# Performance work log

Measured on AMD Instinct MI355X. Metric: run time of the kernel, lower is better.

The kernel has to match this reference:

```python
import jax, jax.numpy as jnp
import numpy as np

N_NODES = 100000
N_EDGES = 1000000
IN_FEATS = 128
HID_FEATS = 128
OUT_FEATS = 128
N_CLASSES = 16
NEG_SLOPE = 0.01
BN_EPS = 1e-5


def _linear_params(key, d_in, d_out):
    k1, k2 = jax.random.split(key)
    s = 1.0 / np.sqrt(d_in)
    w = jax.random.uniform(k1, (d_in, d_out), jnp.float32, -s, s)
    b = jax.random.uniform(k2, (d_out,), jnp.float32, -s, s)
    return w, b


def setup_inputs() -> dict:
    key = jax.random.key(0)
    ks = jax.random.split(key, 16)
    node_feat = jax.random.normal(ks[0], (N_NODES, IN_FEATS), jnp.float32)
    src = jax.random.randint(ks[1], (N_EDGES,), 0, N_NODES, jnp.int32)
    dst = jax.random.randint(ks[2], (N_EDGES,), 0, N_NODES, jnp.int32)
    dims = [(IN_FEATS, HID_FEATS), (HID_FEATS, HID_FEATS), (HID_FEATS, OUT_FEATS)]
    inp = {"node_feat": node_feat, "src": src, "dst": dst}
    for i, (din, dout) in enumerate(dims):
        wp, bp = _linear_params(ks[3 + 4 * i], din, din)      # fc_pool: d_in -> d_in
        ws, _ = _linear_params(ks[4 + 4 * i], din, dout)       # fc_self (no bias)
        wn, _ = _linear_params(ks[5 + 4 * i], din, dout)       # fc_neigh (no bias)
        _, b = _linear_params(ks[6 + 4 * i], din, dout)        # shared output bias
        inp[f"wp{i}"] = wp; inp[f"bp{i}"] = bp
        inp[f"ws{i}"] = ws; inp[f"wn{i}"] = wn; inp[f"b{i}"] = b
    inp["bn_gamma"] = jnp.ones((HID_FEATS,), jnp.float32)
    inp["bn_beta"] = jnp.zeros((HID_FEATS,), jnp.float32)
    wc, bc = _linear_params(ks[15], OUT_FEATS, N_CLASSES)
    inp["wc"] = wc; inp["bc"] = bc
    return inp


def _sage_pool(h, src, dst, deg_mask, wp, bp, ws, wn, b):
    # fc_pool + relu on source nodes, gather per edge, segment-max to dst
    hp = jax.nn.relu(h @ wp + bp)                 # [N, d_in]
    msg = hp[src]                                 # [E, d_in]
    agg = jax.ops.segment_max(msg, dst, num_segments=N_NODES)  # [N, d_in]
    agg = jnp.where(deg_mask, agg, 0.0)           # zero for isolated nodes
    return h @ ws + agg @ wn + b


def _batchnorm(x, gamma, beta):
    mu = jnp.mean(x, axis=0)
    var = jnp.var(x, axis=0)
    return (x - mu) * jax.lax.rsqrt(var + BN_EPS) * gamma + beta


def reference(node_feat, src, dst,
              wp0, bp0, ws0, wn0, b0,
              wp1, bp1, ws1, wn1, b1,
              wp2, bp2, ws2, wn2, b2,
              bn_gamma, bn_beta, wc, bc):
    deg = jnp.zeros((N_NODES,), jnp.float32).at[dst].add(1.0)
    deg_mask = (deg > 0)[:, None]
    h = jax.nn.leaky_relu(_sage_pool(node_feat, src, dst, deg_mask, wp0, bp0, ws0, wn0, b0), NEG_SLOPE)
    h = jax.nn.leaky_relu(_batchnorm(_sage_pool(h, src, dst, deg_mask, wp1, bp1, ws1, wn1, b1), bn_gamma, bn_beta), NEG_SLOPE)
    h = _sage_pool(h, src, dst, deg_mask, wp2, bp2, ws2, wn2, b2)
    return h @ wc + bc
```

## Files before the change

### kernel.cpp

```cpp
#include <hip/hip_runtime.h>


#define N_NODES 100000
#define N_EDGES 1000000
#define F 128
#define NEG_SLOPE 0.01f
#define BN_EPS 1e-5f

typedef __attribute__((ext_vector_type(8))) short bf16x8;
typedef __attribute__((ext_vector_type(4))) float f32x4;

typedef __attribute__((address_space(3))) unsigned int as3_uint;
typedef __attribute__((address_space(1))) const unsigned int as1_cuint;

__device__ __forceinline__ void gload16(const void* g, void* l) {
    __builtin_amdgcn_global_load_lds((as1_cuint*)g, (as3_uint*)l, 16, 0, 0);
}

__device__ __forceinline__ unsigned short f2bf(float f) {
    unsigned int u = __float_as_uint(f);
    u += 0x7fff + ((u >> 16) & 1);
    return (unsigned short)(u >> 16);
}
__device__ __forceinline__ float bf2f(unsigned short h) {
    return __uint_as_float(((unsigned int)h) << 16);
}

__global__ __launch_bounds__(256) void zero_kernel(float4* __restrict__ p, long n4) {
    long i = (long)blockIdx.x * 256 + threadIdx.x;
    if (i < n4) p[i] = make_float4(0.f, 0.f, 0.f, 0.f);
}

__global__ __launch_bounds__(256) void f32_to_bf16_kernel(
    const float4* __restrict__ in, uint2* __restrict__ out, long n4)
{
    long i = (long)blockIdx.x * 256 + threadIdx.x;
    if (i >= n4) return;
    float4 v = in[i];
    uint2 o;
    o.x = (unsigned)f2bf(v.x) | ((unsigned)f2bf(v.y) << 16);
    o.y = (unsigned)f2bf(v.z) | ((unsigned)f2bf(v.w) << 16);
    out[i] = o;
}

__global__ __launch_bounds__(256) void pack_weights3(
    const float* __restrict__ wp, const float* __restrict__ wss,
    const float* __restrict__ wn, short* __restrict__ wp_p, short* __restrict__ wsn_p)
{
    const int i = blockIdx.x * 256 + threadIdx.x;
    if (i >= 3 * 16384) return;
    const int mat = i >> 14;
    const int idx = i & 16383;
    const int k = idx >> 7, n = idx & 127;
    const float* srcm = mat == 0 ? wp : (mat == 1 ? wss : wn);
    const int slot = ((k >> 3) * 128 + n) * 8 + (k & 7);
    if (mat == 0) wp_p[slot] = (short)f2bf(srcm[idx]);
    else wsn_p[(mat == 2 ? 16 * 128 * 8 : 0) + slot] = (short)f2bf(srcm[idx]);
}

template<int NKS>
__global__ __launch_bounds__(256) void gemm_mfma(
    const short* __restrict__ A1, const short* __restrict__ A2,
    const short* __restrict__ Bp, const float* __restrict__ bias,
    unsigned short* __restrict__ Cout, int n_rows, int act)
{
    constexpr int S = NKS / 2;
    __shared__ short tile[2 * 8192];
    __shared__ short epi[4 * 1280];

    const int tid = threadIdx.x;
    const int wave = tid >> 6;
    const int lane = tid & 63;
    const int m = lane & 15, q = lane >> 4;
    const int r0 = blockIdx.x * 128;
    const int rw = (wave >> 1) * 64;
    const int r0q = r0 + rw;
    const int c0 = (wave & 1) * 64;
    const int gchunk = (tid & 7) ^ ((tid >> 3) & 7);

    f32x4 acc[4][4];
#pragma unroll
    for (int i = 0; i < 4; ++i)
#pragma unroll
        for (int j = 0; j < 4; ++j)
#pragma unroll
            for (int r = 0; r < 4; ++r) acc[i][j][r] = 0.f;

    auto stage = [&](int s, int buf) {
        const short* Ap = (NKS == 8 && s >= 2) ? A2 : A1;
        const int kbase = (s & 1) * 64;
#pragma unroll
        for (int p = 0; p < 4; ++p) {
            int row = r0 + (tid >> 3) + 32 * p;
            row = min(row, n_rows - 1);
            gload16(Ap + (size_t)row * F + kbase + gchunk * 8,
                    &tile[buf * 8192 + p * 2048 + tid * 8]);
        }
    };

    stage(0, 0);
    __syncthreads();

    for (int s = 0; s < S; ++s) {
        if (s + 1 < S) stage(s + 1, (s + 1) & 1);
        const short* tb = &tile[(s & 1) * 8192];
#pragma unroll
        for (int ks2 = 0; ks2 < 2; ++ks2) {
            const int ks32 = s * 2 + ks2;
            bf16x8 b[4], a[4];
#pragma unroll
            for (int ni = 0; ni < 4; ++ni)
                b[ni] = *(const bf16x8*)(Bp + ((size_t)(ks32 * 4 + q) * F + c0 + ni * 16 + m) * 8);
#pragma unroll
            for (int mi = 0; mi < 4; ++mi)
                a[mi] = *(const bf16x8*)(tb + (rw + mi * 16 + m) * 64 + (((ks2 * 4 + q) ^ (m & 7)) << 3));
#pragma unroll
            for (int mi = 0; mi < 4; ++mi)
#pragma unroll
                for (int ni = 0; ni < 4; ++ni)
                    acc[mi][ni] = __builtin_amdgcn_mfma_f32_16x16x32_bf16(a[mi], b[ni], acc[mi][ni], 0, 0, 0);
        }
        __syncthreads();
    }

    float bv[4];
#pragma unroll
    for (int ni = 0; ni < 4; ++ni) bv[ni] = bias[c0 + ni * 16 + m];

    short* ep = &epi[wave * 1280];
    const int colc_lo = m >> 3, cin = m & 7;
#pragma unroll
    for (int mi = 0; mi < 4; ++mi) {
#pragma unroll
        for (int ni = 0; ni < 4; ++ni) {
            const int colc = 2 * ni + colc_lo;
#pragma unroll
            for (int rg = 0; rg < 4; ++rg) {
                const int row16 = q * 4 + rg;
                float v = acc[mi][ni][rg] + bv[ni];
                if (act == 1) v = v > 0.f ? v : 0.f;
                else if (act == 2) v = v > 0.f ? v : v * NEG_SLOPE;
                ep[row16 * 80 + ((colc ^ (row16 & 7)) << 3) + cin] = (short)f2bf(v);
            }
        }
        __syncthreads();
#pragma unroll
        for (int p = 0; p < 2; ++p) {
            const int lrow = (lane >> 3) + 8 * p;
            bf16x8 vv = *(const bf16x8*)&ep[lrow * 80 + (((lane & 7) ^ (lrow & 7)) << 3)];
            const int grow = r0q + mi * 16 + lrow;
            if (grow < n_rows)
                *(bf16x8*)(Cout + (size_t)grow * F + c0 + ((lane & 7) << 3)) = vv;
        }
        __syncthreads();
    }
}

__global__ __launch_bounds__(256) void hist_kernel(const int* __restrict__ dst, int* __restrict__ deg) {
    const int e = blockIdx.x * 256 + threadIdx.x;
    if (e < N_EDGES) atomicAdd(&deg[__builtin_nontemporal_load(&dst[e])], 1);
}

__global__ __launch_bounds__(256) void scan1_kernel(const int* __restrict__ deg, int* __restrict__ bsum) {
    __shared__ int sh[256];
    const int t = threadIdx.x;
    const int base = blockIdx.x * 1024 + t * 4;
    int s = 0;
#pragma unroll
    for (int j = 0; j < 4; ++j) s += (base + j < N_NODES) ? deg[base + j] : 0;
    sh[t] = s; __syncthreads();
    for (int off = 128; off; off >>= 1) {
        if (t < off) sh[t] += sh[t + off];
        __syncthreads();
    }
    if (t == 0) bsum[blockIdx.x] = sh[0];
}

__global__ __launch_bounds__(128) void scan2_kernel(int* __restrict__ bsum, int nb, int* __restrict__ row_start) {
    __shared__ int sh[128];
    const int t = threadIdx.x;
    sh[t] = (t < nb) ? bsum[t] : 0;
    __syncthreads();
    for (int off = 1; off < 128; off <<= 1) {
        int x = (t >= off) ? sh[t - off] : 0;
        __syncthreads();
        if (t >= off) sh[t] += x;
        __syncthreads();
    }
    if (t < nb) bsum[t] = t ? sh[t - 1] : 0;
    if (t == 0) row_start[N_NODES] = N_EDGES;
}

__global__ __launch_bounds__(256) void scan3_kernel(
    const int* __restrict__ deg, const int* __restrict__ boff,
    int* __restrict__ row_start, int* __restrict__ cursor)
{
    __shared__ int sh[256];
    const int t = threadIdx.x;
    const int base = blockIdx.x * 1024 + t * 4;
    int v[4]; int s = 0;
#pragma unroll
    for (int j = 0; j < 4; ++j) { v[j] = (base + j < N_NODES) ? deg[base + j] : 0; s += v[j]; }
    sh[t] = s; __syncthreads();
    for (int off = 1; off < 256; off <<= 1) {
        int x = (t >= off) ? sh[t - off] : 0;
        __syncthreads();
        if (t >= off) sh[t] += x;
        __syncthreads();
    }
    int excl = (t ? sh[t - 1] : 0) + boff[blockIdx.x];
#pragma unroll
    for (int j = 0; j < 4; ++j) {
        if (base + j < N_NODES) { row_start[base + j] = excl; cursor[base + j] = excl; }
        excl += v[j];
    }
}

#define NODES_PER_XCD 12500
__global__ __launch_bounds__(256) void scatter_xcd_kernel(
    const int* __restrict__ src, const int* __restrict__ dst,
    int* __restrict__ cursor, int* __restrict__ esrc)
{
    const int range = blockIdx.x & 7;
    const int chunk = blockIdx.x >> 3;
    const int lo = range * NODES_PER_XCD;
    const int e0 = chunk * 3907;
    const int e1 = min(e0 + 3907, N_EDGES);
    for (int e = e0 + threadIdx.x; e < e1; e += 256) {
        const int d = dst[e];
        const unsigned int rel = (unsigned int)(d - lo);
        if (rel < NODES_PER_XCD) {
            const int pos = atomicAdd(&cursor[d], 1);
            esrc[pos] = src[e];
        }
    }
}

__global__ __launch_bounds__(256) void aggregate_max_bf16(
    const unsigned int* __restrict__ hp, const int* __restrict__ row_start,
    const int* __restrict__ esrc, unsigned int* __restrict__ agg)
{
    const int node = blockIdx.x * 4 + (threadIdx.x >> 6);
    if (node >= N_NODES) return;
    const int lane = threadIdx.x & 63;
    const int beg = row_start[node], end = row_start[node + 1];
    unsigned int m0 = 0, m1 = 0;
    int i = beg;
    for (; i + 7 < end; i += 8) {
        unsigned int v[8];
#pragma unroll
        for (int j = 0; j < 8; ++j) v[j] = hp[(size_t)esrc[i + j] * 64 + lane];
#pragma unroll
        for (int j = 0; j < 8; ++j) {
            m0 = max(m0, v[j] & 0xffffu);
            m1 = max(m1, v[j] >> 16);
        }
    }
    if (i + 3 < end) {
        unsigned int v[4];
#pragma unroll
        for (int j = 0; j < 4; ++j) v[j] = hp[(size_t)esrc[i + j] * 64 + lane];
#pragma unroll
        for (int j = 0; j < 4; ++j) {
            m0 = max(m0, v[j] & 0xffffu);
            m1 = max(m1, v[j] >> 16);
        }
        i += 4;
    }
    if (i + 1 < end) {
        const unsigned int a = hp[(size_t)esrc[i] * 64 + lane];
        const unsigned int b = hp[(size_t)esrc[i + 1] * 64 + lane];
        m0 = max(m0, max(a & 0xffffu, b & 0xffffu));
        m1 = max(m1, max(a >> 16, b >> 16));
        i += 2;
    }
    if (i < end) {
        const unsigned int a = hp[(size_t)esrc[i] * 64 + lane];
        m0 = max(m0, a & 0xffffu);
        m1 = max(m1, a >> 16);
    }
    agg[(size_t)node * 64 + lane] = m0 | (m1 << 16);
}

#define BN_ROWS_PER_BLOCK 196
__global__ __launch_bounds__(256) void bn_stats_kernel(
    const unsigned short* __restrict__ x, float* __restrict__ stats, int n)
{
    const int tid = threadIdx.x;
    const int wave = tid >> 6, lane = tid & 63;
    const int rgrp = lane >> 4;
    const int c16 = lane & 15;
    const int rbase = blockIdx.x * BN_ROWS_PER_BLOCK;
    const int rend = min(rbase + BN_ROWS_PER_BLOCK, n);

    float s[8], ss[8];
#pragma unroll
    for (int j = 0; j < 8; ++j) { s[j] = 0.f; ss[j] = 0.f; }

    for (int r = rbase + wave * 4 + rgrp; r < rend; r += 16) {
        const uint4 v = *(const uint4*)(x + (size_t)r * F + c16 * 8);
        const unsigned int w[4] = {v.x, v.y, v.z, v.w};
#pragma unroll
        for (int u = 0; u < 4; ++u) {
            const float f0 = bf2f((unsigned short)(w[u] & 0xffffu));
            const float f1 = bf2f((unsigned short)(w[u] >> 16));
            s[2*u]   += f0; ss[2*u]   = fmaf(f0, f0, ss[2*u]);
            s[2*u+1] += f1; ss[2*u+1] = fmaf(f1, f1, ss[2*u+1]);
        }
    }
#pragma unroll
    for (int j = 0; j < 8; ++j) {
        s[j]  += __shfl_down(s[j], 32);  s[j]  += __shfl_down(s[j], 16);
        ss[j] += __shfl_down(ss[j], 32); ss[j] += __shfl_down(ss[j], 16);
    }
    __shared__ float sh[4][16][16];
    if (lane < 16) {
#pragma unroll
        for (int j = 0; j < 8; ++j) {
            sh[wave][c16][2*j]     = s[j];
            sh[wave][c16][2*j + 1] = ss[j];
        }
    }
    __syncthreads();
    const float tot = sh[0][tid >> 4][tid & 15] + sh[1][tid >> 4][tid & 15]
                    + sh[2][tid >> 4][tid & 15] + sh[3][tid >> 4][tid & 15];
    const int col = (tid >> 4) * 8 + ((tid >> 1) & 7);
    atomicAdd(&stats[(tid & 1) * 128 + col], tot);
}

__global__ void bn_finalize_kernel(
    const float* __restrict__ stats, const float* __restrict__ gamma,
    const float* __restrict__ beta, float* __restrict__ coef)
{
    const int c = threadIdx.x;
    const float mean = stats[c] * (1.f / N_NODES);
    const float var = stats[128 + c] * (1.f / N_NODES) - mean * mean;
    const float scale = gamma[c] * rsqrtf(var + BN_EPS);
    coef[c] = scale;
    coef[128 + c] = fmaf(-mean, scale, beta[c]);
}

__global__ __launch_bounds__(256) void bn_apply_bf16(
    unsigned int* __restrict__ x, const float* __restrict__ coef, long n2)
{
    __shared__ float sc[128], sf[128];
    if (threadIdx.x < 128) {
        sc[threadIdx.x] = coef[threadIdx.x];
        sf[threadIdx.x] = coef[128 + threadIdx.x];
    }
    __syncthreads();
    const long i = (long)blockIdx.x * 256 + threadIdx.x;
    if (i >= n2) return;
    const unsigned int v = x[i];
    const int c0 = (int)(i & 63) * 2;
    float a = fmaf(bf2f((unsigned short)(v & 0xffffu)), sc[c0], sf[c0]);
    float b = fmaf(bf2f((unsigned short)(v >> 16)), sc[c0 + 1], sf[c0 + 1]);
    a = a > 0.f ? a : a * NEG_SLOPE;
    b = b > 0.f ? b : b * NEG_SLOPE;
    x[i] = (unsigned)f2bf(a) | ((unsigned)f2bf(b) << 16);
}

__global__ __launch_bounds__(256) void classifier_kernel(
    const unsigned short* __restrict__ X, const float* __restrict__ Wc,
    const float* __restrict__ bc, float* __restrict__ out, int n)
{
    __shared__ float Wl[2048];
    __shared__ float Xs[16 * 132];
    const int tid = threadIdx.x;
    for (int i = tid; i < 2048; i += 256) Wl[i] = Wc[i];
    const int r0 = blockIdx.x * 16;
    for (int i = tid; i < 2048; i += 256) {
        const int row = i >> 7, col = i & 127;
        const int gr = r0 + row;
        Xs[row * 132 + col] = (gr < n) ? bf2f(X[(size_t)gr * F + col]) : 0.f;
    }
    __syncthreads();
    const int rl = tid >> 4, c = tid & 15;
    const int r = r0 + rl;
    if (r >= n) return;
    float s = bc[c];
    const float* xr = &Xs[rl * 132];
#pragma unroll
    for (int k = 0; k < 128; ++k) s = fmaf(xr[k], Wl[k * 16 + c], s);
    out[(size_t)r * 16 + c] = s;
}

extern "C" void kernel_launch(void* const* d_in, const int* in_sizes, int n_in,
                              void* d_out, int out_size, void* d_ws, size_t ws_size,
                              hipStream_t stream) {
    const float* node_feat = (const float*)d_in[0];
    const int* src = (const int*)d_in[1];
    const int* dst = (const int*)d_in[2];
    const float* wp[3] = {(const float*)d_in[3],  (const float*)d_in[8],  (const float*)d_in[13]};
    const float* bp[3] = {(const float*)d_in[4],  (const float*)d_in[9],  (const float*)d_in[14]};
    const float* wsm[3] = {(const float*)d_in[5], (const float*)d_in[10], (const float*)d_in[15]};
    const float* wn[3] = {(const float*)d_in[6],  (const float*)d_in[11], (const float*)d_in[16]};
    const float* bb[3] = {(const float*)d_in[7],  (const float*)d_in[12], (const float*)d_in[17]};
    const float* gamma = (const float*)d_in[18];
    const float* beta  = (const float*)d_in[19];
    const float* wc    = (const float*)d_in[20];
    const float* bc    = (const float*)d_in[21];

    const size_t SZ = (size_t)N_NODES * F;
    short* sbase = (short*)d_ws;
    short* B0  = sbase;
    short* B1  = sbase + SZ;
    short* B2  = sbase + 2 * SZ;
    short* Xbf = sbase + 3 * SZ;
    short* wp_p  = sbase + 4 * SZ;
    short* wsn_p = wp_p + 3 * 16384;
    float* fbase = (float*)(wsn_p + 3 * 32768);
    float* stats = fbase;
    float* coef  = fbase + 256;
    int* ibase = (int*)(fbase + 512);
    int* deg       = ibase;
    int* row_start = ibase + 100000;
    int* cursor    = ibase + 200104;
    int* esrc      = ibase + 300104;
    int* bsum      = ibase + 1300104;

    const int gGemm = (N_NODES + 127) / 128;
    const int gE    = (N_EDGES + 255) / 256;
    const int gScan = (N_NODES + 1023) / 1024;
    const int gAgg  = (N_NODES + 3) / 4;
    const long cvt4 = (long)(SZ / 4);
    const long n2   = (long)(SZ / 2);

    f32_to_bf16_kernel<<<(int)((cvt4 + 255) / 256), 256, 0, stream>>>(
        (const float4*)node_feat, (uint2*)Xbf, cvt4);
    for (int l = 0; l < 3; ++l)
        pack_weights3<<<192, 256, 0, stream>>>(wp[l], wsm[l], wn[l],
                                               wp_p + l * 16384, wsn_p + l * 32768);

    zero_kernel<<<98, 256, 0, stream>>>((float4*)deg, 25000);
    hist_kernel<<<gE, 256, 0, stream>>>(dst, deg);
    scan1_kernel<<<gScan, 256, 0, stream>>>(deg, bsum);
    scan2_kernel<<<1, 128, 0, stream>>>(bsum, gScan, row_start);
    scan3_kernel<<<gScan, 256, 0, stream>>>(deg, bsum, row_start, cursor);
    scatter_xcd_kernel<<<2048, 256, 0, stream>>>(src, dst, cursor, esrc);

    const short* Xl[3]  = {Xbf, B0, B1};
    short* hpb[3]       = {B0, B1, B0};
    short* aggb[3]      = {B1, B2, B2};
    short* Yb[3]        = {B0, B1, B0};
    for (int l = 0; l < 3; ++l) {
        const short* X = Xl[l];
        gemm_mfma<4><<<gGemm, 256, 0, stream>>>(X, (const short*)nullptr,
            wp_p + l * 16384, bp[l], (unsigned short*)hpb[l], N_NODES, 1);
        aggregate_max_bf16<<<gAgg, 256, 0, stream>>>(
            (const unsigned int*)hpb[l], row_start, esrc, (unsigned int*)aggb[l]);
        const int act = (l == 0) ? 2 : 0;
        gemm_mfma<8><<<gGemm, 256, 0, stream>>>(X, aggb[l],
            wsn_p + l * 32768, bb[l], (unsigned short*)Yb[l], N_NODES, act);
        if (l == 1) {
            zero_kernel<<<1, 256, 0, stream>>>((float4*)stats, 64);
            bn_stats_kernel<<<512, 256, 0, stream>>>(
                (const unsigned short*)Yb[l], stats, N_NODES);
            bn_finalize_kernel<<<1, 128, 0, stream>>>(stats, gamma, beta, coef);
            bn_apply_bf16<<<(int)((n2 + 255) / 256), 256, 0, stream>>>(
                (unsigned int*)Yb[l], coef, n2);
        }
    }
    classifier_kernel<<<(N_NODES + 15) / 16, 256, 0, stream>>>(
        (const unsigned short*)B0, wc, bc, (float*)d_out, N_NODES);
}
```

Measured before the change: 557.4 us.

## Route degree histogram and CSR scatter through XCD-local dynamic work queues

The degree histogram and the edge scatter now read the hardware XCC id and take edge chunks from per-node-range atomic work queues. Each block starts on the node range that matches its own XCD and then steals from the other ranges. The aim is to keep atomics on deg and cursor inside one XCD's L2 rather than relying on blockIdx-to-XCD placement. The GEMM epilogue also reuses the main LDS tile instead of a separate buffer, which lowers LDS use per block. The cost is a queue atomic and two barriers per chunk, plus each block rescanning dst once for every range it works on.

```diff
diff --git a/kernel.cpp b/kernel.cpp
--- a/kernel.cpp
+++ b/kernel.cpp
@@ -6,6 +6,9 @@
 #define F 128
 #define NEG_SLOPE 0.01f
 #define BN_EPS 1e-5f
+#define NODES_PER_XCD 12500
+#define NCHUNK 256
+#define CHUNK_E 3907
 
 typedef __attribute__((ext_vector_type(8))) short bf16x8;
 typedef __attribute__((ext_vector_type(4))) float f32x4;
@@ -15,6 +18,12 @@
 
 __device__ __forceinline__ void gload16(const void* g, void* l) {
     __builtin_amdgcn_global_load_lds((as1_cuint*)g, (as3_uint*)l, 16, 0, 0);
+}
+
+__device__ __forceinline__ int get_xcc_id() {
+    unsigned int x;
+    asm volatile("s_getreg_b32 %0, hwreg(HW_REG_XCC_ID)" : "=s"(x));
+    return (int)(x & 7);
 }
 
 __device__ __forceinline__ unsigned short f2bf(float f) {
@@ -66,7 +75,6 @@
 {
     constexpr int S = NKS / 2;
     __shared__ short tile[2 * 8192];
-    __shared__ short epi[4 * 1280];
 
     const int tid = threadIdx.x;
     const int wave = tid >> 6;
@@ -127,7 +135,7 @@
 #pragma unroll
     for (int ni = 0; ni < 4; ++ni) bv[ni] = bias[c0 + ni * 16 + m];
 
-    short* ep = &epi[wave * 1280];
+    short* ep = &tile[wave * 1280];
     const int colc_lo = m >> 3, cin = m & 7;
 #pragma unroll
     for (int mi = 0; mi < 4; ++mi) {
@@ -156,9 +164,56 @@
     }
 }
 
-__global__ __launch_bounds__(256) void hist_kernel(const int* __restrict__ dst, int* __restrict__ deg) {
-    const int e = blockIdx.x * 256 + threadIdx.x;
-    if (e < N_EDGES) atomicAdd(&deg[__builtin_nontemporal_load(&dst[e])], 1);
+__global__ __launch_bounds__(256) void hist_xcd_kernel(
+    const int* __restrict__ dst, int* __restrict__ deg, int* __restrict__ q)
+{
+    __shared__ int chunk_s;
+    const int my = get_xcc_id();
+    for (int off = 0; off < 8; ++off) {
+        const int r = (my + off) & 7;
+        const int lo = r * NODES_PER_XCD;
+        for (;;) {
+            if (threadIdx.x == 0) chunk_s = atomicAdd(&q[r], 1);
+            __syncthreads();
+            const int chunk = chunk_s;
+            __syncthreads();
+            if (chunk >= NCHUNK) break;
+            const int e0 = chunk * CHUNK_E;
+            const int e1 = min(e0 + CHUNK_E, N_EDGES);
+            for (int e = e0 + threadIdx.x; e < e1; e += 256) {
+                const int d = dst[e];
+                if ((unsigned)(d - lo) < NODES_PER_XCD) atomicAdd(&deg[d], 1);
+            }
+        }
+    }
+}
+
+__global__ __launch_bounds__(256) void scatter_xcd_kernel(
+    const int* __restrict__ src, const int* __restrict__ dst,
+    int* __restrict__ cursor, int* __restrict__ esrc, int* __restrict__ q)
+{
+    __shared__ int chunk_s;
+    const int my = get_xcc_id();
+    for (int off = 0; off < 8; ++off) {
+        const int r = (my + off) & 7;
+        const int lo = r * NODES_PER_XCD;
+        for (;;) {
+            if (threadIdx.x == 0) chunk_s = atomicAdd(&q[r], 1);
+            __syncthreads();
+            const int chunk = chunk_s;
+            __syncthreads();
+            if (chunk >= NCHUNK) break;
+            const int e0 = chunk * CHUNK_E;
+            const int e1 = min(e0 + CHUNK_E, N_EDGES);
+            for (int e = e0 + threadIdx.x; e < e1; e += 256) {
+                const int d = dst[e];
+                if ((unsigned)(d - lo) < NODES_PER_XCD) {
+                    const int pos = atomicAdd(&cursor[d], 1);
+                    esrc[pos] = src[e];
+                }
+            }
+        }
+    }
 }
 
 __global__ __launch_bounds__(256) void scan1_kernel(const int* __restrict__ deg, int* __restrict__ bsum) {
@@ -213,26 +268,6 @@
     for (int j = 0; j < 4; ++j) {
         if (base + j < N_NODES) { row_start[base + j] = excl; cursor[base + j] = excl; }
         excl += v[j];
-    }
-}
-
-#define NODES_PER_XCD 12500
-__global__ __launch_bounds__(256) void scatter_xcd_kernel(
-    const int* __restrict__ src, const int* __restrict__ dst,
-    int* __restrict__ cursor, int* __restrict__ esrc)
-{
-    const int range = blockIdx.x & 7;
-    const int chunk = blockIdx.x >> 3;
-    const int lo = range * NODES_PER_XCD;
-    const int e0 = chunk * 3907;
-    const int e1 = min(e0 + 3907, N_EDGES);
-    for (int e = e0 + threadIdx.x; e < e1; e += 256) {
-        const int d = dst[e];
-        const unsigned int rel = (unsigned int)(d - lo);
-        if (rel < NODES_PER_XCD) {
-            const int pos = atomicAdd(&cursor[d], 1);
-            esrc[pos] = src[e];
-        }
     }
 }
 
@@ -418,9 +453,10 @@
     int* cursor    = ibase + 200104;
     int* esrc      = ibase + 300104;
     int* bsum      = ibase + 1300104;
+    int* qh        = ibase + 1300232;
+    int* qs        = ibase + 1300240;
 
     const int gGemm = (N_NODES + 127) / 128;
-    const int gE    = (N_EDGES + 255) / 256;
     const int gScan = (N_NODES + 1023) / 1024;
     const int gAgg  = (N_NODES + 3) / 4;
     const long cvt4 = (long)(SZ / 4);
@@ -433,11 +469,12 @@
                                                wp_p + l * 16384, wsn_p + l * 32768);
 
     zero_kernel<<<98, 256, 0, stream>>>((float4*)deg, 25000);
-    hist_kernel<<<gE, 256, 0, stream>>>(dst, deg);
+    zero_kernel<<<1, 256, 0, stream>>>((float4*)qh, 4);
+    hist_xcd_kernel<<<2048, 256, 0, stream>>>(dst, deg, qh);
     scan1_kernel<<<gScan, 256, 0, stream>>>(deg, bsum);
     scan2_kernel<<<1, 128, 0, stream>>>(bsum, gScan, row_start);
     scan3_kernel<<<gScan, 256, 0, stream>>>(deg, bsum, row_start, cursor);
-    scatter_xcd_kernel<<<2048, 256, 0, stream>>>(src, dst, cursor, esrc);
+    scatter_xcd_kernel<<<2048, 256, 0, stream>>>(src, dst, cursor, esrc, qs);
 
     const short* Xl[3]  = {Xbf, B0, B1};
     short* hpb[3]       = {B0, B1, B0};
```

New measurement: 957.1 us. 71.7% more time.
